# Kernel tuning notes

Measured on AMD Instinct MI355X. Metric: run time of the kernel, lower is better.

## Reference

```python
import jax, jax.numpy as jnp
import numpy as np

EPS = 1e-6
NUM_ITERS = 8
TEMPERATURE = 1.0


def setup_inputs() -> dict:
    key = jax.random.key(0)
    k1, k2 = jax.random.split(key)
    x = jax.random.normal(k1, (4, 8192, 4096), dtype=jnp.float32)
    # nn.Linear(dim, num_experts, bias=False) weight: [num_experts, dim]
    w_gate = jax.random.normal(k2, (64, 4096), dtype=jnp.float32) * (1.0 / np.sqrt(4096))
    return {"x": x, "w_gate": w_gate}


def sinkhorn(t, num_iters=NUM_ITERS, temperature=TEMPERATURE, eps=EPS):
    # t: [b, n, e] raw gate logits (pre-log)
    t = jnp.log(jnp.clip(t, eps))  # log(clamp(t, min=eps))
    t = t / temperature
    for _ in range(num_iters):
        t = t - jax.nn.logsumexp(t, axis=-2, keepdims=True)  # normalize over tokens
        t = t - jax.nn.logsumexp(t, axis=-1, keepdims=True)  # normalize over experts
    return jnp.exp(t)


def reference(x, w_gate):
    # gate projection: [b, n, d] @ [e, d]^T -> [b, n, e]
    gates = jnp.einsum('bnd,ed->bne', x, w_gate)
    return sinkhorn(gates)
```

## Files before the change

### kernel.cpp

```cpp
#include <hip/hip_runtime.h>
#include <hip/hip_fp16.h>

#define B_ 4
#define N_ 8192
#define D_ 4096
#define E_ 64
#define M_ (B_ * N_)
#define NK 64

typedef _Float16 half8 __attribute__((ext_vector_type(8)));
typedef float f32x4 __attribute__((ext_vector_type(4)));

union H4 { _Float16 h[4]; uint2 u2; };

__global__ __launch_bounds__(256) void convert_w(const float* __restrict__ w,
                                                 _Float16* __restrict__ w16) {
  const int i = (blockIdx.x * 256 + threadIdx.x) * 4;
  const float4 v = *(const float4*)&w[i];
  H4 h;
  h.h[0] = (_Float16)v.x; h.h[1] = (_Float16)v.y;
  h.h[2] = (_Float16)v.z; h.h[3] = (_Float16)v.w;
  *(uint2*)&w16[i] = h.u2;
}

__global__ __launch_bounds__(512, 4) void gemm_log(const float* __restrict__ x,
                                                   const _Float16* __restrict__ w16,
                                                   float* __restrict__ t0,
                                                   float* __restrict__ slot0) {
  __shared__ _Float16 As[2][64 * 64];
  __shared__ float wsum[8][32];

  const int tid = threadIdx.x;
  const int lane = tid & 63;
  const int wv = tid >> 6;
  const int wm = (wv >> 1) * 16;
  const int wn = (wv & 1) * 32;
  const int l15 = lane & 15;
  const int lq = lane >> 4;
  const int rowBase = blockIdx.x * 64;
  const int b = rowBase >> 13;

  const int sr = tid >> 3;
  const int su = tid & 7;
  const float* xs = x + (size_t)(rowBase + sr) * D_ + su * 8;
  const int sdst = sr * 64 + ((su ^ (sr & 7)) << 3);

  const int arow = wm + l15;
  const int aoff0 = arow * 64 + (((0 * 4 + lq) ^ (arow & 7)) << 3);
  const int aoff1 = arow * 64 + (((1 * 4 + lq) ^ (arow & 7)) << 3);

  const _Float16* wB0 = w16 + (size_t)(wn + l15) * D_ + lq * 8;
  const _Float16* wB1 = w16 + (size_t)(wn + 16 + l15) * D_ + lq * 8;

  f32x4 acc0 = {}, acc1 = {};
  float4 xa, xb;
  half8 b00, b01, b10, b11;

  xa = *(const float4*)(xs);
  xb = *(const float4*)(xs + 4);

  for (int kc = 0; kc < NK; ++kc) {
    const int cur = kc & 1;
    const int ko = kc * 64;

    b00 = *(const half8*)(wB0 + ko);
    b01 = *(const half8*)(wB0 + ko + 32);
    b10 = *(const half8*)(wB1 + ko);
    b11 = *(const half8*)(wB1 + ko + 32);

    half8 hx;
    hx[0] = (_Float16)xa.x; hx[1] = (_Float16)xa.y;
    hx[2] = (_Float16)xa.z; hx[3] = (_Float16)xa.w;
    hx[4] = (_Float16)xb.x; hx[5] = (_Float16)xb.y;
    hx[6] = (_Float16)xb.z; hx[7] = (_Float16)xb.w;
    *(half8*)&As[cur][sdst] = hx;

    if (kc + 1 < NK) {
      xa = *(const float4*)(xs + ko + 64);
      xb = *(const float4*)(xs + ko + 68);
    }

    asm volatile("s_waitcnt lgkmcnt(0)" ::: "memory");
    __builtin_amdgcn_s_barrier();

    half8 a0 = *(const half8*)&As[cur][aoff0];
    half8 a1 = *(const half8*)&As[cur][aoff1];
    acc0 = __builtin_amdgcn_mfma_f32_16x16x32_f16(a0, b00, acc0, 0, 0, 0);
    acc0 = __builtin_amdgcn_mfma_f32_16x16x32_f16(a1, b01, acc0, 0, 0, 0);
    acc1 = __builtin_amdgcn_mfma_f32_16x16x32_f16(a0, b10, acc1, 0, 0, 0);
    acc1 = __builtin_amdgcn_mfma_f32_16x16x32_f16(a1, b11, acc1, 0, 0, 0);
  }

  float ls0 = 0.f, ls1 = 0.f;
#pragma unroll
  for (int r = 0; r < 4; ++r) {
    const float v0 = fmaxf(acc0[r], 1e-6f);
    const float v1 = fmaxf(acc1[r], 1e-6f);
    const int grow = rowBase + wm + lq * 4 + r;
    t0[(size_t)grow * E_ + wn + l15] = __logf(v0);
    t0[(size_t)grow * E_ + wn + 16 + l15] = __logf(v1);
    ls0 += v0; ls1 += v1;
  }
  {
    float vv = ls0;
    vv += __shfl_xor(vv, 16); vv += __shfl_xor(vv, 32);
    if (lq == 0) wsum[wv][l15] = vv;
    vv = ls1;
    vv += __shfl_xor(vv, 16); vv += __shfl_xor(vv, 32);
    if (lq == 0) wsum[wv][16 + l15] = vv;
  }
  __syncthreads();
  if (tid < 64) {
    const int e = tid;
    const int half = e >> 5;
    const int idx = e & 31;
    const float tot = wsum[0 * 2 + half][idx] + wsum[1 * 2 + half][idx] +
                      wsum[2 * 2 + half][idx] + wsum[3 * 2 + half][idx];
    atomicAdd(&slot0[b * E_ + e], tot);
  }
}

__global__ __launch_bounds__(256) void sinkhorn_iter(const float* __restrict__ t0,
                                                     float* __restrict__ slots,
                                                     float* __restrict__ out,
                                                     int it, int last) {
  const int tid = threadIdx.x;
  const int lane = tid & 63;
  const int wv = tid >> 6;
  const int b = blockIdx.x >> 8;
  const int chunk = blockIdx.x & 255;

  float C = __logf(slots[b * E_ + lane]);
  for (int j = 1; j < it; ++j) C += __logf(slots[j * (B_ * E_) + b * E_ + lane]);

  float colacc = 0.f;
  const int nbase = chunk * 32 + wv * 8;
#pragma unroll
  for (int i = 0; i < 8; ++i) {
    const int n = nbase + i;
    const float v = t0[((size_t)b * N_ + n) * E_ + lane];
    const float p = __expf(v - C);
    float s = p;
    s += __shfl_xor(s, 1);  s += __shfl_xor(s, 2);  s += __shfl_xor(s, 4);
    s += __shfl_xor(s, 8);  s += __shfl_xor(s, 16); s += __shfl_xor(s, 32);
    const float q = p / s;
    if (last) out[((size_t)b * N_ + n) * E_ + lane] = q;
    else      colacc += q;
  }
  if (!last) {
    __shared__ float wsum[4][64];
    wsum[wv][lane] = colacc;
    __syncthreads();
    if (tid < 64) {
      const float tot = wsum[0][tid] + wsum[1][tid] + wsum[2][tid] + wsum[3][tid];
      atomicAdd(&slots[it * (B_ * E_) + b * E_ + tid], tot);
    }
  }
}

extern "C" void kernel_launch(void* const* d_in, const int* in_sizes, int n_in,
                              void* d_out, int out_size, void* d_ws, size_t ws_size,
                              hipStream_t stream) {
  (void)in_sizes; (void)n_in; (void)out_size; (void)ws_size;
  const float* x = (const float*)d_in[0];
  const float* w = (const float*)d_in[1];
  float* out = (float*)d_out;
  float* slots = (float*)d_ws;
  _Float16* w16 = (_Float16*)((char*)d_ws + 8192);

  hipMemsetAsync(slots, 0, 8 * B_ * E_ * sizeof(float), stream);
  convert_w<<<(E_ * D_) / 1024, 256, 0, stream>>>(w, w16);
  gemm_log<<<M_ / 64, 512, 0, stream>>>(x, w16, out, slots);
  for (int it = 1; it <= 8; ++it)
    sinkhorn_iter<<<B_ * 256, 256, 0, stream>>>(out, slots, out, it, it == 8 ? 1 : 0);
}
```

Measured before the change: 253.6 us.

## Stage W tiles through LDS and deepen global prefetch to two chunks

The gate weight chunk is now loaded cooperatively, once per block, into a swizzled LDS buffer instead of each wave fetching its own B fragments straight from global memory. The K loop is unrolled by two with separate register sets, so global loads for x and W are issued two chunks ahead of their use. This aims to cut redundant global/L2 traffic for W and hide memory latency better. It adds 16 KB of LDS and more registers per thread, which may reduce occupancy under the 512x4 launch bounds.

```diff
diff --git a/kernel.cpp b/kernel.cpp
--- a/kernel.cpp
+++ b/kernel.cpp
@@ -28,6 +28,7 @@
                                                    float* __restrict__ t0,
                                                    float* __restrict__ slot0) {
   __shared__ _Float16 As[2][64 * 64];
+  __shared__ _Float16 Bs[2][64 * 64];
   __shared__ float wsum[8][32];
 
   const int tid = threadIdx.x;
@@ -43,52 +44,60 @@
   const int sr = tid >> 3;
   const int su = tid & 7;
   const float* xs = x + (size_t)(rowBase + sr) * D_ + su * 8;
+  const _Float16* ws = w16 + (size_t)sr * D_ + su * 8;
   const int sdst = sr * 64 + ((su ^ (sr & 7)) << 3);
 
   const int arow = wm + l15;
-  const int aoff0 = arow * 64 + (((0 * 4 + lq) ^ (arow & 7)) << 3);
-  const int aoff1 = arow * 64 + (((1 * 4 + lq) ^ (arow & 7)) << 3);
-
-  const _Float16* wB0 = w16 + (size_t)(wn + l15) * D_ + lq * 8;
-  const _Float16* wB1 = w16 + (size_t)(wn + 16 + l15) * D_ + lq * 8;
+  const int aoff0 = arow * 64 + ((lq ^ (arow & 7)) << 3);
+  const int aoff1 = arow * 64 + (((4 + lq) ^ (arow & 7)) << 3);
+  const int bcol0 = wn + l15;
+  const int bcol1 = wn + 16 + l15;
+  const int boff00 = bcol0 * 64 + ((lq ^ (bcol0 & 7)) << 3);
+  const int boff01 = bcol0 * 64 + (((4 + lq) ^ (bcol0 & 7)) << 3);
+  const int boff10 = bcol1 * 64 + ((lq ^ (bcol1 & 7)) << 3);
+  const int boff11 = bcol1 * 64 + (((4 + lq) ^ (bcol1 & 7)) << 3);
 
   f32x4 acc0 = {}, acc1 = {};
-  float4 xa, xb;
-  half8 b00, b01, b10, b11;
 
-  xa = *(const float4*)(xs);
-  xb = *(const float4*)(xs + 4);
+  float4 ax0, ax1, cx0, cx1;
+  half8 abw, cbw;
 
-  for (int kc = 0; kc < NK; ++kc) {
-    const int cur = kc & 1;
-    const int ko = kc * 64;
-
-    b00 = *(const half8*)(wB0 + ko);
-    b01 = *(const half8*)(wB0 + ko + 32);
-    b10 = *(const half8*)(wB1 + ko);
-    b11 = *(const half8*)(wB1 + ko + 32);
-
+  auto body = [&](float4& px0, float4& px1, half8& pbw, int buf, int kpref) {
     half8 hx;
-    hx[0] = (_Float16)xa.x; hx[1] = (_Float16)xa.y;
-    hx[2] = (_Float16)xa.z; hx[3] = (_Float16)xa.w;
-    hx[4] = (_Float16)xb.x; hx[5] = (_Float16)xb.y;
-    hx[6] = (_Float16)xb.z; hx[7] = (_Float16)xb.w;
-    *(half8*)&As[cur][sdst] = hx;
-
-    if (kc + 1 < NK) {
-      xa = *(const float4*)(xs + ko + 64);
-      xb = *(const float4*)(xs + ko + 68);
+    hx[0] = (_Float16)px0.x; hx[1] = (_Float16)px0.y;
+    hx[2] = (_Float16)px0.z; hx[3] = (_Float16)px0.w;
+    hx[4] = (_Float16)px1.x; hx[5] = (_Float16)px1.y;
+    hx[6] = (_Float16)px1.z; hx[7] = (_Float16)px1.w;
+    *(half8*)&As[buf][sdst] = hx;
+    *(half8*)&Bs[buf][sdst] = pbw;
+    if (kpref < NK) {
+      const int o = kpref * 64;
+      px0 = *(const float4*)(xs + o);
+      px1 = *(const float4*)(xs + o + 4);
+      pbw = *(const half8*)(ws + o);
     }
-
     asm volatile("s_waitcnt lgkmcnt(0)" ::: "memory");
     __builtin_amdgcn_s_barrier();
-
-    half8 a0 = *(const half8*)&As[cur][aoff0];
-    half8 a1 = *(const half8*)&As[cur][aoff1];
+    half8 a0  = *(const half8*)&As[buf][aoff0];
+    half8 a1  = *(const half8*)&As[buf][aoff1];
+    half8 b00 = *(const half8*)&Bs[buf][boff00];
+    half8 b01 = *(const half8*)&Bs[buf][boff01];
+    half8 b10 = *(const half8*)&Bs[buf][boff10];
+    half8 b11 = *(const half8*)&Bs[buf][boff11];
     acc0 = __builtin_amdgcn_mfma_f32_16x16x32_f16(a0, b00, acc0, 0, 0, 0);
     acc0 = __builtin_amdgcn_mfma_f32_16x16x32_f16(a1, b01, acc0, 0, 0, 0);
     acc1 = __builtin_amdgcn_mfma_f32_16x16x32_f16(a0, b10, acc1, 0, 0, 0);
     acc1 = __builtin_amdgcn_mfma_f32_16x16x32_f16(a1, b11, acc1, 0, 0, 0);
+  };
+
+  ax0 = *(const float4*)(xs);      ax1 = *(const float4*)(xs + 4);
+  abw = *(const half8*)(ws);
+  cx0 = *(const float4*)(xs + 64); cx1 = *(const float4*)(xs + 68);
+  cbw = *(const half8*)(ws + 64);
+
+  for (int kc = 0; kc < NK; kc += 2) {
+    body(ax0, ax1, abw, 0, kc + 2);
+    body(cx0, cx1, cbw, 1, kc + 3);
   }
 
   float ls0 = 0.f, ls1 = 0.f;
```

After: 241.6 us. 4.8% less time.
